# Performance work log

Hardware: AMD Instinct MI355X
Metric: run time of the kernel (lower is better)

Reference implementation:

```python
import jax, jax.numpy as jnp
import numpy as np

WS, OWS, NHEAD = 4, 6, 6          # window, overlap window = 4 + int(0.5*4), heads
B, CIN, COU, H, W = 2, 192, 192, 224, 224
MID = CIN  # r = 1


def calc_rpi_oca(ws=WS, ows=OWS):
    # relative position index between ws x ws query window and ows x ows overlapping kv window
    co = np.stack(np.meshgrid(np.arange(ws), np.arange(ws), indexing='ij')).reshape(2, -1)
    ce = np.stack(np.meshgrid(np.arange(ows), np.arange(ows), indexing='ij')).reshape(2, -1)
    rel = (ce[:, None, :] - co[:, :, None]).transpose(1, 2, 0) + (ws - 1)  # [ws*ws, ows*ows, 2], >= 0
    idx = rel[..., 0] * (ws + ows - 1) + rel[..., 1]                       # in [0, (ws+ows-1)^2)
    return jnp.asarray(idx)  # [16, 36]

RPI = calc_rpi_oca()


def conv2d(x, w, b, pad):
    out = jax.lax.conv_general_dilated(x, w, (1, 1), [(pad, pad), (pad, pad)],
                                       dimension_numbers=('NCHW', 'OIHW', 'NCHW'))
    return out + b[None, :, None, None]


def group_norm(x, g, b, groups, eps=1e-5):
    n = x.shape[0]
    xg = x.reshape(n, groups, -1)
    mu = xg.mean(-1, keepdims=True)
    var = xg.var(-1, keepdims=True)
    xn = ((xg - mu) * jax.lax.rsqrt(var + eps)).reshape(x.shape)
    return xn * g[None, :, None, None] + b[None, :, None, None]


def layer_norm(x, g, b, eps=1e-5):
    mu = x.mean(-1, keepdims=True)
    var = x.var(-1, keepdims=True)
    return (x - mu) * jax.lax.rsqrt(var + eps) * g + b


def ocab(x, h, w, ln1_g, ln1_b, qkv_w, qkv_b, rpb, proj_w, proj_b,
         ln2_g, ln2_b, fc1_w, fc1_b, fc2_w, fc2_b):
    b, _, c = x.shape
    nh, nw, d = h // WS, w // WS, c // NHEAD
    shortcut = x
    xn = layer_norm(x, ln1_g, ln1_b).reshape(b, h, w, c)
    qkv = xn @ qkv_w + qkv_b                                  # [b,h,w,3c] laid out [q|k|v]
    q = qkv[..., :c]
    kv = jnp.stack([qkv[..., c:2 * c], qkv[..., 2 * c:]])     # [2,b,h,w,c]
    # non-overlapping query windows -> [b*nwin, 16, NHEAD, d]
    qw = q.reshape(b, nh, WS, nw, WS, c).transpose(0, 1, 3, 2, 4, 5).reshape(b * nh * nw, WS * WS, NHEAD, d)
    # overlapping kv windows = Unfold(kernel=OWS, stride=WS, pad=(OWS-WS)//2)
    pad = (OWS - WS) // 2
    kvp = jnp.pad(kv, ((0, 0), (0, 0), (pad, pad), (pad, pad), (0, 0)))
    rows = (jnp.arange(nh) * WS)[:, None] + jnp.arange(OWS)[None, :]   # [nh, OWS]
    cols = (jnp.arange(nw) * WS)[:, None] + jnp.arange(OWS)[None, :]   # [nw, OWS]
    patches = kvp[:, :, rows[:, None, :, None], cols[None, :, None, :], :]  # [2,b,nh,nw,OWS,OWS,c]
    kvw = patches.reshape(2, b * nh * nw, OWS * OWS, NHEAD, d)
    kw, vw = kvw[0], kvw[1]
    attn = jnp.einsum('wqhd,wkhd->whqk', qw * (d ** -0.5), kw)  # [b*nwin, NHEAD, 16, 36]
    bias = rpb[RPI.reshape(-1)].reshape(WS * WS, OWS * OWS, NHEAD).transpose(2, 0, 1)
    attn = jax.nn.softmax(attn + bias[None], axis=-1)
    out = jnp.einsum('whqk,wkhd->wqhd', attn, vw).reshape(b, nh, nw, WS, WS, c)
    out = out.transpose(0, 1, 3, 2, 4, 5).reshape(b, h * w, c)  # window_reverse
    out = out @ proj_w + proj_b + shortcut
    xm = layer_norm(out, ln2_g, ln2_b)
    mlp = jax.nn.gelu(xm @ fc1_w + fc1_b, approximate=False) @ fc2_w + fc2_b
    return out + mlp


def atoca_forward(x, conv1_w, conv1_b, gn1_g, gn1_b, conv2_w, conv2_b, gn2_g, gn2_b,
                  conv3_w, conv3_b, ln1_g, ln1_b, qkv_w, qkv_b, rpb, proj_w, proj_b,
                  ln2_g, ln2_b, fc1_w, fc1_b, fc2_w, fc2_b):
    Bx, C, Hx, Wx = x.shape
    shortcut = x
    # raw row-major reshape, exactly as the torch code (not a spatial window partition)
    out = x.reshape(Bx * (Hx // WS) * (Wx // WS), C, WS, WS)
    out = conv2d(out, conv1_w, conv1_b, 1)
    out = jax.nn.silu(group_norm(out, gn1_g, gn1_b, NHEAD))
    out = out.transpose(0, 2, 3, 1).reshape(Bx, Hx * Wx, -1)
    out = ocab(out, Hx, Wx, ln1_g, ln1_b, qkv_w, qkv_b, rpb, proj_w, proj_b,
               ln2_g, ln2_b, fc1_w, fc1_b, fc2_w, fc2_b)
    out = out.reshape(Bx * (Hx // WS) * (Wx // WS), WS, WS, -1).transpose(0, 3, 1, 2)
    out = conv2d(out, conv2_w, conv2_b, 1)
    out = group_norm(out, gn2_g, gn2_b, NHEAD)
    out = out.reshape(Bx, -1, Hx, Wx)
    out = out + conv2d(shortcut, conv3_w, conv3_b, 0)
    return jax.nn.relu(out)


def setup_inputs() -> dict:
    key = jax.random.key(0)
    ks = iter(jax.random.split(key, 32))
    rn = lambda shape, s=0.02: (s * jax.random.normal(next(ks), shape)).astype(jnp.float32)
    return {
        'x': jax.random.normal(next(ks), (B, CIN, H, W), dtype=jnp.float32),
        'conv1_w': rn((MID, CIN, 3, 3)), 'conv1_b': rn((MID,)),
        'gn1_g': jnp.ones((MID,), jnp.float32), 'gn1_b': jnp.zeros((MID,), jnp.float32),
        'conv2_w': rn((COU, MID, 3, 3)), 'conv2_b': rn((COU,)),
        'gn2_g': jnp.ones((COU,), jnp.float32), 'gn2_b': jnp.zeros((COU,), jnp.float32),
        'conv3_w': rn((COU, CIN, 1, 1)), 'conv3_b': rn((COU,)),
        'ln1_g': jnp.ones((MID,), jnp.float32), 'ln1_b': jnp.zeros((MID,), jnp.float32),
        'qkv_w': rn((MID, 3 * MID)), 'qkv_b': rn((3 * MID,)),
        'rpb': rn(((WS + OWS - 1) ** 2, NHEAD)),
        'proj_w': rn((MID, MID)), 'proj_b': rn((MID,)),
        'ln2_g': jnp.ones((MID,), jnp.float32), 'ln2_b': jnp.zeros((MID,), jnp.float32),
        'fc1_w': rn((MID, 2 * MID)), 'fc1_b': rn((2 * MID,)),
        'fc2_w': rn((2 * MID, MID)), 'fc2_b': rn((MID,)),
    }


def reference(x, conv1_w, conv1_b, gn1_g, gn1_b, conv2_w, conv2_b, gn2_g, gn2_b,
              conv3_w, conv3_b, ln1_g, ln1_b, qkv_w, qkv_b, rpb, proj_w, proj_b,
              ln2_g, ln2_b, fc1_w, fc1_b, fc2_w, fc2_b):
    return atoca_forward(x, conv1_w, conv1_b, gn1_g, gn1_b, conv2_w, conv2_b, gn2_g, gn2_b,
                         conv3_w, conv3_b, ln1_g, ln1_b, qkv_w, qkv_b, rpb, proj_w, proj_b,
                         ln2_g, ln2_b, fc1_w, fc1_b, fc2_w, fc2_b)
```

## Files before the change

### kernel.cpp

```cpp
#include <hip/hip_runtime.h>
#include <hip/hip_bf16.h>
#include <math.h>

typedef __hip_bfloat16 bf16;
typedef __attribute__((ext_vector_type(8))) short s8v;
typedef __attribute__((ext_vector_type(4))) short s4v;
typedef __attribute__((ext_vector_type(4))) float f32x4;
typedef __attribute__((ext_vector_type(2))) _Float16 h2;

constexpr int CB   = 2;
constexpr int CH   = 224, CW = 224;
constexpr int NHW  = 56;
constexpr int NPATCH = CB * NHW * NHW;
constexpr int TOKPB  = CH * CW;
constexpr int MTOK   = CB * TOKPB;
constexpr size_t SECSZ = 19267584;

constexpr size_t B_T0  = 0;
constexpr size_t B_P2  = B_T0 + 38535168;
constexpr size_t B_P3  = B_P2 + 115605504;
constexpr size_t B_P4  = B_P3 + 38535168;
constexpr size_t B_WF1 = B_P4 + 38535168;
constexpr size_t B_WF2 = B_WF1 + 1327104;
constexpr size_t B_W3F = B_WF2 + 1327104;
constexpr size_t B_WQ  = B_W3F + 147456;
constexpr size_t B_WP  = B_WQ + 221184;
constexpr size_t B_WG1 = B_WP + 73728;
constexpr size_t B_WG2 = B_WG1 + 147456;
constexpr size_t WS_NEEDED = B_WG2 + 147456;

__device__ __forceinline__ float ldf(const float* p) { return *p; }
__device__ __forceinline__ float ldf(const bf16* p)  { return __bfloat162float(*p); }
__device__ __forceinline__ void  stf(float* p, float v) { *p = v; }
__device__ __forceinline__ void  stf(bf16* p, float v)  { *p = __float2bfloat16(v); }
__device__ __forceinline__ unsigned short f2bf(float f) {
    unsigned u = __builtin_bit_cast(unsigned, f);
    unsigned r = (u + 0x7fffu + ((u >> 16) & 1u)) >> 16;
    return (unsigned short)r;
}
__device__ __forceinline__ float bf2f(short s) {
    unsigned u = ((unsigned)(unsigned short)s) << 16;
    return __builtin_bit_cast(float, u);
}

__global__ void build_wf_kernel(const float* __restrict__ w, short* __restrict__ wf) {
    int o = blockIdx.x * 256 + threadIdx.x;
    if (o >= 331776) return;
    int within = o & 511, frag = o >> 9;
    int l = within >> 3, j = within & 7;
    int nt = frag % 12, t2 = frag / 12, ks = t2 % 6, tap = t2 / 6;
    int co = nt * 16 + (l & 15);
    int ci = ks * 32 + (l >> 4) * 8 + j;
    wf[o] = (short)f2bf(w[(co * 192 + ci) * 9 + tap]);
}
__global__ void build_wgemm_kernel(const float* __restrict__ w, short* __restrict__ wf,
                                   int K, int N) {
    int o = blockIdx.x * 256 + threadIdx.x;
    if (o >= K * N) return;
    int j = o & 7, l = (o >> 3) & 63, f = o >> 9;
    int ntiles = N >> 4;
    int kt = f / ntiles, nt = f % ntiles;
    int k = kt * 32 + (l >> 4) * 8 + j;
    int col = nt * 16 + (l & 15);
    wf[o] = (short)f2bf(w[(size_t)k * N + col]);
}
__global__ void build_w3f_kernel(const float* __restrict__ w, short* __restrict__ wf) {
    int o = blockIdx.x * 256 + threadIdx.x;
    if (o >= 36864) return;
    int j = o & 7, l = (o >> 3) & 63, f = o >> 9;
    int kt = f / 12, ct = f % 12;
    int co = ct * 16 + (l & 15);
    int ci = kt * 32 + (l >> 4) * 8 + j;
    wf[o] = (short)f2bf(w[co * 192 + ci]);
}

template <bool FIRST>
__global__ __launch_bounds__(256, 4) void conv_mfma_kernel(
    const void* __restrict__ srcv, const short* __restrict__ wf,
    const float* __restrict__ bias, const float* __restrict__ gng,
    const float* __restrict__ gnb, bf16* __restrict__ dst)
{
    __shared__ short xs[13056];
    __shared__ float gsum[4][6], gsum2[4][6], gmu[4][6], grs[4][6];
    const int tid  = threadIdx.x;
    const int lane = tid & 63, wid = tid >> 6;
    const int n0   = blockIdx.x * 4;

    if (tid < 24) { gsum[tid / 6][tid % 6] = 0.f; gsum2[tid / 6][tid % 6] = 0.f; }
    for (int u = tid; u < 4 * 192; u += 256) {
        int q = u / 192;
        xs[q * 3264 + 3072 + (u % 192)] = 0;
    }

    if constexpr (FIRST) {
        const float4* sp = (const float4*)((const float*)srcv + (size_t)n0 * 3072);
        #pragma unroll
        for (int u = 0; u < 12; ++u) {
            int idx = u * 256 + tid;
            float4 v = sp[idx];
            int q = idx / 768;
            int li = (idx % 768) * 4;
            int ci = li >> 4, p0 = li & 15;
            float vv[4] = { v.x, v.y, v.z, v.w };
            #pragma unroll
            for (int k = 0; k < 4; ++k) {
                int row = p0 + k;
                int ba = q * 6528 + ((row * 384 + ci * 2) ^ ((row & 7) << 4));
                *(short*)((char*)xs + ba) = (short)f2bf(vv[k]);
            }
        }
    } else {
        const s8v* sp8 = (const s8v*)((const bf16*)srcv + (size_t)n0 * 3072);
        #pragma unroll
        for (int u = 0; u < 6; ++u) {
            int li = u * 256 + tid;
            int r = li / 24, ch = li % 24;
            int q = r >> 4, rl = r & 15;
            s8v val = sp8[li];
            int ba = q * 6528 + ((rl * 384 + ch * 16) ^ ((rl & 7) << 4));
            *(s8v*)((char*)xs + ba) = val;
        }
    }
    __syncthreads();

    const int ntb = wid * 3;
    const int cl  = lane & 15;
    const int kg  = lane >> 4;
    f32x4 acc[3][4];
    #pragma unroll
    for (int t = 0; t < 3; ++t) {
        float bv = bias[(ntb + t) * 16 + cl];
        #pragma unroll
        for (int q = 0; q < 4; ++q) acc[t][q] = (f32x4){ bv, bv, bv, bv };
    }

    const int pi = cl >> 2, pj = cl & 3;
    const s8v* wf8 = (const s8v*)wf;

    for (int tap = 0; tap < 9; ++tap) {
        const int di = tap / 3, dj = tap % 3;
        const int ii = pi + di - 1, jj = pj + dj - 1;
        const bool valid = (ii >= 0 && ii < 4 && jj >= 0 && jj < 4);
        const int nr  = valid ? (ii * 4 + jj) : 16;
        const int rb  = nr * 384;
        const int swz = (nr & 7) << 4;
        #pragma unroll
        for (int ks = 0; ks < 6; ++ks) {
            const s8v* bp = wf8 + (size_t)((tap * 6 + ks) * 12) * 64 + lane;
            s8v b0 = bp[(ntb + 0) * 64];
            s8v b1 = bp[(ntb + 1) * 64];
            s8v b2 = bp[(ntb + 2) * 64];
            const int inner = (rb + ks * 64 + kg * 16) ^ swz;
            #pragma unroll
            for (int q = 0; q < 4; ++q) {
                s8v a = *(const s8v*)((const char*)xs + q * 6528 + inner);
                acc[0][q] = __builtin_amdgcn_mfma_f32_16x16x32_bf16(a, b0, acc[0][q], 0, 0, 0);
                acc[1][q] = __builtin_amdgcn_mfma_f32_16x16x32_bf16(a, b1, acc[1][q], 0, 0, 0);
                acc[2][q] = __builtin_amdgcn_mfma_f32_16x16x32_bf16(a, b2, acc[2][q], 0, 0, 0);
            }
        }
    }

    #pragma unroll
    for (int t = 0; t < 3; ++t) {
        const int g = (ntb + t) >> 1;
        #pragma unroll
        for (int q = 0; q < 4; ++q) {
            f32x4 A = acc[t][q];
            float s  = A[0] + A[1] + A[2] + A[3];
            float s2 = A[0]*A[0] + A[1]*A[1] + A[2]*A[2] + A[3]*A[3];
            #pragma unroll
            for (int off = 32; off; off >>= 1) { s += __shfl_xor(s, off); s2 += __shfl_xor(s2, off); }
            if (lane == 0) { atomicAdd(&gsum[q][g], s); atomicAdd(&gsum2[q][g], s2); }
        }
    }
    __syncthreads();
    if (tid < 24) {
        int q = tid / 6, g = tid % 6;
        float mu  = gsum[q][g] * (1.f / 512.f);
        float var = gsum2[q][g] * (1.f / 512.f) - mu * mu;
        gmu[q][g] = mu; grs[q][g] = rsqrtf(var + 1e-5f);
    }
    __syncthreads();

    if constexpr (FIRST) {
        #pragma unroll
        for (int t = 0; t < 3; ++t) {
            const int co = (ntb + t) * 16 + cl, g = (ntb + t) >> 1;
            const float gg = gng[co], gb = gnb[co];
            #pragma unroll
            for (int q = 0; q < 4; ++q) {
                const float mu = gmu[q][g], rs = grs[q][g];
                #pragma unroll
                for (int r = 0; r < 4; ++r) {
                    float v = (acc[t][q][r] - mu) * rs * gg + gb;
                    v = v / (1.f + __expf(-v));
                    int row = q * 16 + kg * 4 + r;
                    int ba = (row * 384 + co * 2) ^ ((row & 7) << 4);
                    *(short*)((char*)xs + ba) = (short)f2bf(v);
                }
            }
        }
        __syncthreads();
        bf16* dp = dst + (size_t)n0 * 3072;
        #pragma unroll
        for (int u = 0; u < 6; ++u) {
            int li = u * 256 + tid;
            int row = li / 24, g2 = li % 24;
            int ba = (row * 384 + g2 * 16) ^ ((row & 7) << 4);
            s8v val = *(const s8v*)((const char*)xs + ba);
            *(s8v*)(dp + (size_t)row * 192 + g2 * 8) = val;
        }
    } else {
        #pragma unroll
        for (int t = 0; t < 3; ++t) {
            const int co = (ntb + t) * 16 + cl, g = (ntb + t) >> 1;
            const float gg = gng[co], gb = gnb[co];
            #pragma unroll
            for (int q = 0; q < 4; ++q) {
                const float mu = gmu[q][g], rs = grs[q][g];
                #pragma unroll
                for (int r = 0; r < 4; ++r) {
                    float v = (acc[t][q][r] - mu) * rs * gg + gb;
                    xs[q * 3072 + co * 16 + kg * 4 + r] = (short)f2bf(v);
                }
            }
        }
        __syncthreads();
        s4v* dp = (s4v*)(dst + (size_t)n0 * 3072);
        const s4v* sps = (const s4v*)xs;
        #pragma unroll
        for (int u = 0; u < 12; ++u) {
            dp[u * 256 + tid] = sps[u * 256 + tid];
        }
    }
}

template <bool RES, bool GELU_ACT, bool LN, bool QKVOUT, int NKT>
__global__ __launch_bounds__(256) void gemm_mfma_kernel(
    const bf16* __restrict__ A, const short* __restrict__ wfb,
    const float* __restrict__ bias, const bf16* __restrict__ res,
    void* __restrict__ out, int N,
    const float* __restrict__ lng, const float* __restrict__ lnb)
{
    __shared__ short ls[8192];
    const int tid = threadIdx.x, lane = tid & 63, wid = tid >> 6;
    const int m0 = blockIdx.x * 128;
    const int cl = lane & 15, kg = lane >> 4;
    constexpr int K = NKT * 32;
    const int ntiles = N >> 4;
    const int ntsec = ntiles / gridDim.y;
    const int ntbeg = blockIdx.y * ntsec;

    s8v af0[NKT], af1[NKT];
    const int r0 = m0 + wid * 32 + cl;
    #pragma unroll
    for (int kt = 0; kt < NKT; ++kt) {
        af0[kt] = *(const s8v*)(A + (size_t)r0 * K + kt * 32 + kg * 8);
        af1[kt] = *(const s8v*)(A + (size_t)(r0 + 16) * K + kt * 32 + kg * 8);
    }
    if constexpr (LN) {
        static_assert(!LN || NKT == 6, "LN requires K==192");
        #pragma unroll
        for (int r = 0; r < 2; ++r) {
            s8v* af = r ? af1 : af0;
            float s = 0.f, s2 = 0.f;
            #pragma unroll
            for (int kt = 0; kt < NKT; ++kt)
                #pragma unroll
                for (int j = 0; j < 8; ++j) {
                    float v = bf2f(af[kt][j]);
                    s += v; s2 += v * v;
                }
            s  += __shfl_xor(s, 16);  s2 += __shfl_xor(s2, 16);
            s  += __shfl_xor(s, 32);  s2 += __shfl_xor(s2, 32);
            const float mu = s * (1.f / 192.f);
            const float rs = rsqrtf(s2 * (1.f / 192.f) - mu * mu + 1e-5f);
            #pragma unroll
            for (int kt = 0; kt < NKT; ++kt) {
                const float* gp = lng + kt * 32 + kg * 8;
                const float* bp = lnb + kt * 32 + kg * 8;
                #pragma unroll
                for (int j = 0; j < 8; ++j) {
                    float v = (bf2f(af[kt][j]) - mu) * rs * gp[j] + bp[j];
                    af[kt][j] = (short)f2bf(v);
                }
            }
        }
    }

    const s8v* wf8 = (const s8v*)wfb;
    for (int nt0 = ntbeg; nt0 < ntbeg + ntsec; nt0 += 4) {
        const int n0 = nt0 * 16;
        f32x4 acc[2][4];
        #pragma unroll
        for (int nf = 0; nf < 4; ++nf) {
            float bv = bias[n0 + nf * 16 + cl];
            acc[0][nf] = (f32x4){ bv, bv, bv, bv };
            acc[1][nf] = (f32x4){ bv, bv, bv, bv };
        }
        #pragma unroll
        for (int kt = 0; kt < NKT; ++kt) {
            #pragma unroll
            for (int nf = 0; nf < 4; ++nf) {
                s8v b = wf8[(size_t)(kt * ntiles + nt0 + nf) * 64 + lane];
                acc[0][nf] = __builtin_amdgcn_mfma_f32_16x16x32_bf16(af0[kt], b, acc[0][nf], 0, 0, 0);
                acc[1][nf] = __builtin_amdgcn_mfma_f32_16x16x32_bf16(af1[kt], b, acc[1][nf], 0, 0, 0);
            }
        }

        __syncthreads();
        #pragma unroll
        for (int rf = 0; rf < 2; ++rf) {
            #pragma unroll
            for (int nf = 0; nf < 4; ++nf) {
                const int lcol = nf * 16 + cl;
                #pragma unroll
                for (int r = 0; r < 4; ++r) {
                    const int lrow = wid * 32 + rf * 16 + kg * 4 + r;
                    float v = acc[rf][nf][r];
                    if (GELU_ACT) v = 0.5f * v * (1.f + erff(v * 0.70710678118f));
                    short sv;
                    if constexpr (QKVOUT) sv = __builtin_bit_cast(short, (_Float16)v);
                    else                  sv = (short)f2bf(v);
                    int ba = (lrow * 128 + lcol * 2) ^ ((lrow & 7) << 4);
                    *(short*)((char*)ls + ba) = sv;
                }
            }
        }
        __syncthreads();
        #pragma unroll
        for (int p = 0; p < 4; ++p) {
            const int lrow = p * 32 + (tid >> 3);
            const int g = tid & 7;
            int ba = (lrow * 128 + g * 16) ^ ((lrow & 7) << 4);
            s8v val = *(const s8v*)((const char*)ls + ba);
            const int row = m0 + lrow;
            const int col0 = n0 + g * 8;
            if constexpr (QKVOUT) {
                const int sec = n0 / 192;
                const int c0 = col0 - sec * 192, h = c0 >> 5, d0 = c0 & 31;
                const int bb2 = row / TOKPB, t = row - bb2 * TOKPB;
                *(s8v*)((_Float16*)out + (size_t)sec * SECSZ +
                        ((size_t)(bb2 * 6 + h) * TOKPB + t) * 32 + d0) = val;
            } else if constexpr (RES) {
                s8v rv = *(const s8v*)(res + (size_t)row * N + col0);
                s8v ov;
                #pragma unroll
                for (int e = 0; e < 8; ++e) ov[e] = (short)f2bf(bf2f(val[e]) + bf2f(rv[e]));
                *(s8v*)((bf16*)out + (size_t)row * N + col0) = ov;
            } else {
                *(s8v*)((bf16*)out + (size_t)row * N + col0) = val;
            }
        }
    }
}

constexpr int HSTR = 1160;
__global__ __launch_bounds__(128) void attn_kernel(
    const _Float16* __restrict__ qf, const float* __restrict__ rpb,
    bf16* __restrict__ out)
{
    __shared__ short kh[6 * HSTR];
    __shared__ short vh[6 * HSTR];
    const int w = blockIdx.x;
    const int b = w / (NHW * NHW), wi = w % (NHW * NHW);
    const int nhi = wi / NHW, nwi = wi % NHW;
    const int tid = threadIdx.x;
    const int r0 = nhi * 4 - 1, c0 = nwi * 4 - 1;
    const _Float16* kfb = qf + SECSZ;
    const _Float16* vfb = qf + 2 * SECSZ;

    #pragma unroll
    for (int it = 0; it < 14; ++it) {
        int v = tid + it * 128;
        if (v < 1728) {
            int kv = v >= 864 ? 1 : 0;
            int u = v - kv * 864;
            int h = u / 144, rem = u % 144, kj = rem >> 2, d0 = (rem & 3) * 8;
            int rr = r0 + kj / 6, cc = c0 + kj % 6;
            s8v val = { 0, 0, 0, 0, 0, 0, 0, 0 };
            if (rr >= 0 && rr < CH && cc >= 0 && cc < CW) {
                const _Float16* src = kv ? vfb : kfb;
                val = *(const s8v*)(src + ((size_t)(b * 6 + h) * TOKPB + rr * CW + cc) * 32 + d0);
            }
            short* dst = kv ? vh : kh;
            *(s8v*)(dst + h * HSTR + kj * 32 + d0) = val;
        }
    }
    __syncthreads();

    if (tid < 96) {
        const int h = tid >> 4, qi = tid & 15;
        const int qr = nhi * 4 + (qi >> 2), qc = nwi * 4 + (qi & 3);
        const _Float16* qp = qf + ((size_t)(b * 6 + h) * TOKPB + qr * CW + qc) * 32;
        h2 qh[16];
        #pragma unroll
        for (int u = 0; u < 4; ++u) {
            uint4 qa = *(const uint4*)(qp + u * 8);
            qh[u * 4 + 0] = __builtin_bit_cast(h2, qa.x);
            qh[u * 4 + 1] = __builtin_bit_cast(h2, qa.y);
            qh[u * 4 + 2] = __builtin_bit_cast(h2, qa.z);
            qh[u * 4 + 3] = __builtin_bit_cast(h2, qa.w);
        }

        float sc[36];
        const short* khb = kh + h * HSTR;
        #pragma unroll
        for (int kj = 0; kj < 36; ++kj) {
            const uint4* kp = (const uint4*)(khb + kj * 32);
            uint4 k0 = kp[0], k1 = kp[1], k2 = kp[2], k3 = kp[3];
            unsigned kwv[16] = { k0.x, k0.y, k0.z, k0.w, k1.x, k1.y, k1.z, k1.w,
                                 k2.x, k2.y, k2.z, k2.w, k3.x, k3.y, k3.z, k3.w };
            float a0 = 0.f, a1 = 0.f, a2 = 0.f, a3 = 0.f;
            #pragma unroll
            for (int e = 0; e < 4; ++e) {
                a0 = __builtin_amdgcn_fdot2(__builtin_bit_cast(h2, kwv[4*e+0]), qh[4*e+0], a0, false);
                a1 = __builtin_amdgcn_fdot2(__builtin_bit_cast(h2, kwv[4*e+1]), qh[4*e+1], a1, false);
                a2 = __builtin_amdgcn_fdot2(__builtin_bit_cast(h2, kwv[4*e+2]), qh[4*e+2], a2, false);
                a3 = __builtin_amdgcn_fdot2(__builtin_bit_cast(h2, kwv[4*e+3]), qh[4*e+3], a3, false);
            }
            const int rel0 = kj / 6 - (qi >> 2) + 3;
            const int rel1 = kj % 6 - (qi & 3) + 3;
            sc[kj] = ((a0 + a1) + (a2 + a3)) * 0.17677669529f + rpb[(rel0 * 9 + rel1) * 6 + h];
        }
        float mx = -1e30f;
        #pragma unroll
        for (int kj = 0; kj < 36; ++kj) mx = fmaxf(mx, sc[kj]);
        float sum = 0.f;
        #pragma unroll
        for (int kj = 0; kj < 36; ++kj) { sc[kj] = __expf(sc[kj] - mx); sum += sc[kj]; }
        const float inv = 1.f / sum;

        h2 o2[16];
        #pragma unroll
        for (int e = 0; e < 16; ++e) o2[e] = (h2){ (_Float16)0.f, (_Float16)0.f };
        const short* vhb = vh + h * HSTR;
        #pragma unroll
        for (int kj = 0; kj < 36; ++kj) {
            const uint4* vp = (const uint4*)(vhb + kj * 32);
            uint4 v0 = vp[0], v1 = vp[1], v2 = vp[2], v3 = vp[3];
            unsigned vwv[16] = { v0.x, v0.y, v0.z, v0.w, v1.x, v1.y, v1.z, v1.w,
                                 v2.x, v2.y, v2.z, v2.w, v3.x, v3.y, v3.z, v3.w };
            const _Float16 ph = (_Float16)sc[kj];
            const h2 ph2 = { ph, ph };
            #pragma unroll
            for (int e = 0; e < 16; ++e)
                o2[e] = __builtin_bit_cast(h2, vwv[e]) * ph2 + o2[e];
        }
        bf16* op = out + ((size_t)(b * TOKPB + qr * CW + qc)) * 192 + h * 32;
        #pragma unroll
        for (int u = 0; u < 8; ++u) {
            s4v pk;
            #pragma unroll
            for (int e = 0; e < 2; ++e) {
                h2 ov = o2[u * 2 + e];
                pk[2 * e]     = (short)f2bf((float)ov[0] * inv);
                pk[2 * e + 1] = (short)f2bf((float)ov[1] * inv);
            }
            *(s4v*)((bf16*)op + u * 4) = pk;
        }
    }
}

__global__ __launch_bounds__(256, 4) void final_mfma_kernel(
    const float* __restrict__ x, const short* __restrict__ w3f,
    const float* __restrict__ b3, const bf16* __restrict__ c2,
    float* __restrict__ out)
{
    __shared__ short xs2[12288];
    const int pix0 = blockIdx.x * 64;
    const int b    = blockIdx.y;
    const int tid = threadIdx.x, lane = tid & 63, wid = tid >> 6;
    const int cl = lane & 15, kg = lane >> 4;
    const float* xb = x + (size_t)b * (192 * TOKPB);

    #pragma unroll
    for (int u = 0; u < 12; ++u) {
        int idx = u * 256 + tid;
        int ci = idx >> 4, p4 = (idx & 15) << 2;
        float4 v = *(const float4*)(xb + (size_t)ci * TOKPB + pix0 + p4);
        float vv[4] = { v.x, v.y, v.z, v.w };
        #pragma unroll
        for (int k = 0; k < 4; ++k) {
            int row = p4 + k;
            int ba = (row * 384 + ci * 2) ^ ((row & 7) << 4);
            *(short*)((char*)xs2 + ba) = (short)f2bf(vv[k]);
        }
    }
    __syncthreads();

    const int ctb = wid * 3;
    f32x4 acc[3][4] = {};
    const s8v* wf8 = (const s8v*)w3f;

    #pragma unroll
    for (int kt = 0; kt < 6; ++kt) {
        s8v a0 = wf8[(size_t)(kt * 12 + ctb + 0) * 64 + lane];
        s8v a1 = wf8[(size_t)(kt * 12 + ctb + 1) * 64 + lane];
        s8v a2 = wf8[(size_t)(kt * 12 + ctb + 2) * 64 + lane];
        #pragma unroll
        for (int pt = 0; pt < 4; ++pt) {
            int row = pt * 16 + cl;
            int ba = (row * 384 + kt * 64 + kg * 16) ^ ((row & 7) << 4);
            s8v bfr = *(const s8v*)((const char*)xs2 + ba);
            acc[0][pt] = __builtin_amdgcn_mfma_f32_16x16x32_bf16(a0, bfr, acc[0][pt], 0, 0, 0);
            acc[1][pt] = __builtin_amdgcn_mfma_f32_16x16x32_bf16(a1, bfr, acc[1][pt], 0, 0, 0);
            acc[2][pt] = __builtin_amdgcn_mfma_f32_16x16x32_bf16(a2, bfr, acc[2][pt], 0, 0, 0);
        }
    }

    #pragma unroll
    for (int t = 0; t < 3; ++t) {
        #pragma unroll
        for (int r = 0; r < 4; ++r) {
            const int co = (ctb + t) * 16 + kg * 4 + r;
            const float bb = b3[co];
            const size_t rowbase = (size_t)b * (192 * TOKPB) + (size_t)co * TOKPB + pix0;
            #pragma unroll
            for (int pt = 0; pt < 4; ++pt) {
                const size_t f = rowbase + pt * 16 + cl;
                float v = acc[t][pt][r] + bb + bf2f(__builtin_bit_cast(short, c2[f]));
                out[f] = fmaxf(v, 0.f);
            }
        }
    }
}

extern "C" void kernel_launch(void* const* d_in, const int* in_sizes, int n_in,
                              void* d_out, int out_size, void* d_ws, size_t ws_size,
                              hipStream_t stream)
{
    if (ws_size < WS_NEEDED) return;

    const float* x       = (const float*)d_in[0];
    const float* conv1_w = (const float*)d_in[1];
    const float* conv1_b = (const float*)d_in[2];
    const float* gn1_g   = (const float*)d_in[3];
    const float* gn1_b   = (const float*)d_in[4];
    const float* conv2_w = (const float*)d_in[5];
    const float* conv2_b = (const float*)d_in[6];
    const float* gn2_g   = (const float*)d_in[7];
    const float* gn2_b   = (const float*)d_in[8];
    const float* conv3_w = (const float*)d_in[9];
    const float* conv3_b = (const float*)d_in[10];
    const float* ln1_g   = (const float*)d_in[11];
    const float* ln1_b   = (const float*)d_in[12];
    const float* qkv_w   = (const float*)d_in[13];
    const float* qkv_b   = (const float*)d_in[14];
    const float* rpb     = (const float*)d_in[15];
    const float* proj_w  = (const float*)d_in[16];
    const float* proj_b  = (const float*)d_in[17];
    const float* ln2_g   = (const float*)d_in[18];
    const float* ln2_b   = (const float*)d_in[19];
    const float* fc1_w   = (const float*)d_in[20];
    const float* fc1_b   = (const float*)d_in[21];
    const float* fc2_w   = (const float*)d_in[22];
    const float* fc2_b   = (const float*)d_in[23];

    char* wsb = (char*)d_ws;
    bf16*  T0  = (bf16*)(wsb + B_T0);
    _Float16* QF = (_Float16*)(wsb + B_P2);
    bf16*  HID = (bf16*)(wsb + B_P2);
    bf16*  P3  = (bf16*)(wsb + B_P3);
    bf16*  P4  = (bf16*)(wsb + B_P4);
    short* WF1 = (short*)(wsb + B_WF1);
    short* WF2 = (short*)(wsb + B_WF2);
    short* W3F = (short*)(wsb + B_W3F);
    short* WQ  = (short*)(wsb + B_WQ);
    short* WP  = (short*)(wsb + B_WP);
    short* WG1 = (short*)(wsb + B_WG1);
    short* WG2 = (short*)(wsb + B_WG2);
    float* OUT = (float*)d_out;

    build_wf_kernel<<<(331776 + 255) / 256, 256, 0, stream>>>(conv1_w, WF1);
    build_wf_kernel<<<(331776 + 255) / 256, 256, 0, stream>>>(conv2_w, WF2);
    build_w3f_kernel<<<(36864 + 255) / 256, 256, 0, stream>>>(conv3_w, W3F);
    build_wgemm_kernel<<<(110592 + 255) / 256, 256, 0, stream>>>(qkv_w, WQ, 192, 576);
    build_wgemm_kernel<<<(36864 + 255) / 256, 256, 0, stream>>>(proj_w, WP, 192, 192);
    build_wgemm_kernel<<<(73728 + 255) / 256, 256, 0, stream>>>(fc1_w, WG1, 192, 384);
    build_wgemm_kernel<<<(73728 + 255) / 256, 256, 0, stream>>>(fc2_w, WG2, 384, 192);

    conv_mfma_kernel<true><<<NPATCH / 4, 256, 0, stream>>>(x, WF1, conv1_b, gn1_g, gn1_b, T0);
    gemm_mfma_kernel<false, false, true, true, 6><<<dim3(MTOK / 128, 3), 256, 0, stream>>>(
        T0, WQ, qkv_b, nullptr, QF, 576, ln1_g, ln1_b);
    attn_kernel<<<NPATCH, 128, 0, stream>>>(QF, rpb, P3);
    gemm_mfma_kernel<true, false, false, false, 6><<<dim3(MTOK / 128, 3), 256, 0, stream>>>(
        P3, WP, proj_b, T0, P4, 192, nullptr, nullptr);
    gemm_mfma_kernel<false, true, true, false, 6><<<dim3(MTOK / 128, 3), 256, 0, stream>>>(
        P4, WG1, fc1_b, nullptr, HID, 384, ln2_g, ln2_b);
    gemm_mfma_kernel<true, false, false, false, 12><<<dim3(MTOK / 128, 3), 256, 0, stream>>>(
        HID, WG2, fc2_b, P4, P3, 192, nullptr, nullptr);
    conv_mfma_kernel<false><<<NPATCH / 4, 256, 0, stream>>>(P3, WF2, conv2_b, gn2_g, gn2_b, P4);
    final_mfma_kernel<<<dim3(TOKPB / 64, CB), 256, 0, stream>>>(x, W3F, conv3_b, P4, OUT);
}
```

Measured before the change: 619.3 us.

## Give each conv wave one full patch and shrink GEMM grids to one column block

The fused conv+GroupNorm kernel now assigns one 4x4 patch to each wave, covering all 12 output-channel tiles, instead of splitting channel tiles across waves. That lets each wave compute GroupNorm statistics with in-wave shuffles alone, removing the shared-memory atomics and one block barrier. The cost is that each wave now loads four times as many weight fragments from global memory while making fewer LDS reads. Separately, the proj, fc1 and fc2 GEMM launches drop from three y-blocks to one, which only stays correct if the GEMM kernel already covers all N columns per block or the extra y-blocks were doing redundant work.

Result: slower. 932.8 us (+50.6%).

```diff
diff --git a/kernel.cpp b/kernel.cpp
--- a/kernel.cpp
+++ b/kernel.cpp
@@ -81,12 +81,10 @@
     const float* __restrict__ gnb, bf16* __restrict__ dst)
 {
     __shared__ short xs[13056];
-    __shared__ float gsum[4][6], gsum2[4][6], gmu[4][6], grs[4][6];
     const int tid  = threadIdx.x;
     const int lane = tid & 63, wid = tid >> 6;
     const int n0   = blockIdx.x * 4;
 
-    if (tid < 24) { gsum[tid / 6][tid % 6] = 0.f; gsum2[tid / 6][tid % 6] = 0.f; }
     for (int u = tid; u < 4 * 192; u += 256) {
         int q = u / 192;
         xs[q * 3264 + 3072 + (u % 192)] = 0;
@@ -123,15 +121,14 @@
     }
     __syncthreads();
 
-    const int ntb = wid * 3;
+    const int q   = wid;
     const int cl  = lane & 15;
     const int kg  = lane >> 4;
-    f32x4 acc[3][4];
-    #pragma unroll
-    for (int t = 0; t < 3; ++t) {
-        float bv = bias[(ntb + t) * 16 + cl];
-        #pragma unroll
-        for (int q = 0; q < 4; ++q) acc[t][q] = (f32x4){ bv, bv, bv, bv };
+    f32x4 acc[12];
+    #pragma unroll
+    for (int t = 0; t < 12; ++t) {
+        float bv = bias[t * 16 + cl];
+        acc[t] = (f32x4){ bv, bv, bv, bv };
     }
 
     const int pi = cl >> 2, pj = cl & 3;
@@ -147,58 +144,43 @@
         #pragma unroll
         for (int ks = 0; ks < 6; ++ks) {
             const s8v* bp = wf8 + (size_t)((tap * 6 + ks) * 12) * 64 + lane;
-            s8v b0 = bp[(ntb + 0) * 64];
-            s8v b1 = bp[(ntb + 1) * 64];
-            s8v b2 = bp[(ntb + 2) * 64];
             const int inner = (rb + ks * 64 + kg * 16) ^ swz;
-            #pragma unroll
-            for (int q = 0; q < 4; ++q) {
-                s8v a = *(const s8v*)((const char*)xs + q * 6528 + inner);
-                acc[0][q] = __builtin_amdgcn_mfma_f32_16x16x32_bf16(a, b0, acc[0][q], 0, 0, 0);
-                acc[1][q] = __builtin_amdgcn_mfma_f32_16x16x32_bf16(a, b1, acc[1][q], 0, 0, 0);
-                acc[2][q] = __builtin_amdgcn_mfma_f32_16x16x32_bf16(a, b2, acc[2][q], 0, 0, 0);
-            }
-        }
-    }
-
-    #pragma unroll
-    for (int t = 0; t < 3; ++t) {
-        const int g = (ntb + t) >> 1;
-        #pragma unroll
-        for (int q = 0; q < 4; ++q) {
-            f32x4 A = acc[t][q];
-            float s  = A[0] + A[1] + A[2] + A[3];
-            float s2 = A[0]*A[0] + A[1]*A[1] + A[2]*A[2] + A[3]*A[3];
-            #pragma unroll
-            for (int off = 32; off; off >>= 1) { s += __shfl_xor(s, off); s2 += __shfl_xor(s2, off); }
-            if (lane == 0) { atomicAdd(&gsum[q][g], s); atomicAdd(&gsum2[q][g], s2); }
-        }
+            s8v a = *(const s8v*)((const char*)xs + q * 6528 + inner);
+            #pragma unroll
+            for (int t = 0; t < 12; ++t) {
+                acc[t] = __builtin_amdgcn_mfma_f32_16x16x32_bf16(a, bp[t * 64], acc[t], 0, 0, 0);
+            }
+        }
+    }
+
+    float mu6[6], rs6[6];
+    #pragma unroll
+    for (int g = 0; g < 6; ++g) {
+        f32x4 A0 = acc[2 * g], A1 = acc[2 * g + 1];
+        float s  = A0[0] + A0[1] + A0[2] + A0[3] + A1[0] + A1[1] + A1[2] + A1[3];
+        float s2 = A0[0]*A0[0] + A0[1]*A0[1] + A0[2]*A0[2] + A0[3]*A0[3]
+                 + A1[0]*A1[0] + A1[1]*A1[1] + A1[2]*A1[2] + A1[3]*A1[3];
+        #pragma unroll
+        for (int off = 32; off; off >>= 1) { s += __shfl_xor(s, off); s2 += __shfl_xor(s2, off); }
+        float mu  = s * (1.f / 512.f);
+        float var = s2 * (1.f / 512.f) - mu * mu;
+        mu6[g] = mu; rs6[g] = rsqrtf(var + 1e-5f);
     }
     __syncthreads();
-    if (tid < 24) {
-        int q = tid / 6, g = tid % 6;
-        float mu  = gsum[q][g] * (1.f / 512.f);
-        float var = gsum2[q][g] * (1.f / 512.f) - mu * mu;
-        gmu[q][g] = mu; grs[q][g] = rsqrtf(var + 1e-5f);
-    }
-    __syncthreads();
 
     if constexpr (FIRST) {
         #pragma unroll
-        for (int t = 0; t < 3; ++t) {
-            const int co = (ntb + t) * 16 + cl, g = (ntb + t) >> 1;
+        for (int t = 0; t < 12; ++t) {
+            const int co = t * 16 + cl, g = t >> 1;
             const float gg = gng[co], gb = gnb[co];
-            #pragma unroll
-            for (int q = 0; q < 4; ++q) {
-                const float mu = gmu[q][g], rs = grs[q][g];
-                #pragma unroll
-                for (int r = 0; r < 4; ++r) {
-                    float v = (acc[t][q][r] - mu) * rs * gg + gb;
-                    v = v / (1.f + __expf(-v));
-                    int row = q * 16 + kg * 4 + r;
-                    int ba = (row * 384 + co * 2) ^ ((row & 7) << 4);
-                    *(short*)((char*)xs + ba) = (short)f2bf(v);
-                }
+            const float mu = mu6[g], rs = rs6[g];
+            #pragma unroll
+            for (int r = 0; r < 4; ++r) {
+                float v = (acc[t][r] - mu) * rs * gg + gb;
+                v = v / (1.f + __expf(-v));
+                int row = q * 16 + kg * 4 + r;
+                int ba = (row * 384 + co * 2) ^ ((row & 7) << 4);
+                *(short*)((char*)xs + ba) = (short)f2bf(v);
             }
         }
         __syncthreads();
@@ -213,17 +195,14 @@
         }
     } else {
         #pragma unroll
-        for (int t = 0; t < 3; ++t) {
-            const int co = (ntb + t) * 16 + cl, g = (ntb + t) >> 1;
+        for (int t = 0; t < 12; ++t) {
+            const int co = t * 16 + cl, g = t >> 1;
             const float gg = gng[co], gb = gnb[co];
-            #pragma unroll
-            for (int q = 0; q < 4; ++q) {
-                const float mu = gmu[q][g], rs = grs[q][g];
-                #pragma unroll
-                for (int r = 0; r < 4; ++r) {
-                    float v = (acc[t][q][r] - mu) * rs * gg + gb;
-                    xs[q * 3072 + co * 16 + kg * 4 + r] = (short)f2bf(v);
-                }
+            const float mu = mu6[g], rs = rs6[g];
+            #pragma unroll
+            for (int r = 0; r < 4; ++r) {
+                float v = (acc[t][r] - mu) * rs * gg + gb;
+                xs[q * 3072 + co * 16 + kg * 4 + r] = (short)f2bf(v);
             }
         }
         __syncthreads();
@@ -585,11 +564,11 @@
     gemm_mfma_kernel<false, false, true, true, 6><<<dim3(MTOK / 128, 3), 256, 0, stream>>>(
         T0, WQ, qkv_b, nullptr, QF, 576, ln1_g, ln1_b);
     attn_kernel<<<NPATCH, 128, 0, stream>>>(QF, rpb, P3);
-    gemm_mfma_kernel<true, false, false, false, 6><<<dim3(MTOK / 128, 3), 256, 0, stream>>>(
+    gemm_mfma_kernel<true, false, false, false, 6><<<dim3(MTOK / 128, 1), 256, 0, stream>>>(
         P3, WP, proj_b, T0, P4, 192, nullptr, nullptr);
-    gemm_mfma_kernel<false, true, true, false, 6><<<dim3(MTOK / 128, 3), 256, 0, stream>>>(
+    gemm_mfma_kernel<false, true, true, false, 6><<<dim3(MTOK / 128, 1), 256, 0, stream>>>(
         P4, WG1, fc1_b, nullptr, HID, 384, ln2_g, ln2_b);
-    gemm_mfma_kernel<true, false, false, false, 12><<<dim3(MTOK / 128, 3), 256, 0, stream>>>(
+    gemm_mfma_kernel<true, false, false, false, 12><<<dim3(MTOK / 128, 1), 256, 0, stream>>>(
         HID, WG2, fc2_b, P4, P3, 192, nullptr, nullptr);
     conv_mfma_kernel<false><<<NPATCH / 4, 256, 0, stream>>>(P3, WF2, conv2_b, gn2_g, gn2_b, P4);
     final_mfma_kernel<<<dim3(TOKPB / 64, CB), 256, 0, stream>>>(x, W3F, conv3_b, P4, OUT);
```
